# Optimization experiments

Hardware: AMD Instinct MI355X
Metric: run time of the kernel (lower is better)

Reference implementation:

```python
import jax, jax.numpy as jnp
import numpy as np

D_MODEL = 1024
N_HEADS = 16
HEAD_DIM = D_MODEL // N_HEADS


def setup_inputs() -> dict:
    key = jax.random.key(0)
    ks = jax.random.split(key, 11)
    B, S = 4, 2048
    scale = 1.0 / np.sqrt(D_MODEL)
    inp = {
        "query": jax.random.normal(ks[0], (B, S, D_MODEL), jnp.float32),
        "key": jax.random.normal(ks[1], (B, S, D_MODEL), jnp.float32),
        "value": jax.random.normal(ks[2], (B, S, D_MODEL), jnp.float32),
        "Wq": jax.random.normal(ks[3], (D_MODEL, D_MODEL), jnp.float32) * scale,
        "bq": jnp.zeros((D_MODEL,), jnp.float32),
        "Wk": jax.random.normal(ks[4], (D_MODEL, D_MODEL), jnp.float32) * scale,
        "bk": jnp.zeros((D_MODEL,), jnp.float32),
        "Wv": jax.random.normal(ks[5], (D_MODEL, D_MODEL), jnp.float32) * scale,
        "bv": jnp.zeros((D_MODEL,), jnp.float32),
        "Wo": jax.random.normal(ks[6], (D_MODEL, D_MODEL), jnp.float32) * scale,
        "bo": jnp.zeros((D_MODEL,), jnp.float32),
    }
    return inp


def reference(query, key, value, Wq, bq, Wk, bk, Wv, bv, Wo, bo):
    B, S, _ = query.shape
    # QKV projections (nn.Linear: x @ W.T + b; weights here stored as [out,in])
    q = query @ Wq.T + bq
    k = key @ Wk.T + bk
    v = value @ Wv.T + bv
    # [B, S, H, Dh] -> [B, H, S, Dh]
    q = q.reshape(B, S, N_HEADS, HEAD_DIM).transpose(0, 2, 1, 3)
    k = k.reshape(B, S, N_HEADS, HEAD_DIM).transpose(0, 2, 1, 3)
    v = v.reshape(B, S, N_HEADS, HEAD_DIM).transpose(0, 2, 1, 3)
    # full score matrix [B, H, S, S]
    scores = jnp.einsum("bhqd,bhkd->bhqk", q, k) / jnp.sqrt(
        jnp.asarray(HEAD_DIM, q.dtype)
    )
    attn = jax.nn.softmax(scores, axis=-1)
    out = jnp.einsum("bhqk,bhkd->bhqd", attn, v)  # [B, H, S, Dh]
    out = out.transpose(0, 2, 1, 3).reshape(B, S, D_MODEL)
    return out @ Wo.T + bo
```

## Files before the change

kernel.cpp:

```cpp
#include <hip/hip_runtime.h>
#include <cstdint>
#include <cstddef>


typedef _Float16 h16;
typedef _Float16 h16x4 __attribute__((ext_vector_type(4)));
typedef _Float16 h16x8 __attribute__((ext_vector_type(8)));
typedef float f32x4 __attribute__((ext_vector_type(4)));
typedef float f32x16 __attribute__((ext_vector_type(16)));

#define SEQ 2048
#define HDIM 64

__device__ __forceinline__ void gld16(const void* g, void* l) {
  __builtin_amdgcn_global_load_lds((__attribute__((address_space(1))) void*)g,
                                   (__attribute__((address_space(3))) void*)l,
                                   16, 0, 0);
}

struct CvtArgs {
  const float* src[7];
  h16* dst[7];
  int n4[7];
};

__global__ __launch_bounds__(256) void cvt_kernel(CvtArgs a) {
  const int tk = blockIdx.y;
  const int n4 = a.n4[tk];
  const float4* s = (const float4*)a.src[tk];
  h16x4* d = (h16x4*)a.dst[tk];
  const int stride = gridDim.x * blockDim.x;
  for (int i = blockIdx.x * blockDim.x + threadIdx.x; i < n4; i += stride) {
    float4 v = s[i];
    h16x4 o = {(h16)v.x, (h16)v.y, (h16)v.z, (h16)v.w};
    d[i] = o;
  }
}

enum { EPI_QK = 0, EPI_V = 1, EPI_OUT = 2 };

struct GemmArgs {
  const h16* A[3];
  const h16* W[3];
  const float* bias[3];
  void* dst[3];
  float scale[3];
  int epi[3];
};

__global__ __launch_bounds__(256) void gemm_h16(GemmArgs g) {
  const int z = blockIdx.z;
  const h16* A = g.A[z];
  const h16* W = g.W[z];
  const float* bias = g.bias[z];
  void* dst = g.dst[z];
  const float scale = g.scale[z];
  const int epi = g.epi[z];

  __shared__ __align__(16) h16 sA[128 * 32];
  __shared__ __align__(16) h16 sW[128 * 32];

  const int t = threadIdx.x;
  const int lane = t & 63, wave = t >> 6;
  const int lq = lane & 15, quad = lane >> 4;
  const int wm = wave & 1, wn = wave >> 1;
  const int m0 = blockIdx.y * 128, n0 = blockIdx.x * 128;

  const int srow = wave * 32 + (lane >> 2);
  const int scol = (lane & 3) * 8;
  const h16* Ag = A + (size_t)(m0 + srow) * 1024 + scol;
  const h16* Wg = W + (size_t)(n0 + srow) * 1024 + scol;
  h16* lA = &sA[(wave * 32) * 32];
  h16* lW = &sW[(wave * 32) * 32];

  f32x4 zero4 = {0.f, 0.f, 0.f, 0.f};
  f32x4 acc[4][4];
#pragma unroll
  for (int i = 0; i < 4; ++i)
#pragma unroll
    for (int j = 0; j < 4; ++j) acc[i][j] = zero4;

  for (int k0 = 0; k0 < 1024; k0 += 32) {
    __syncthreads();
    gld16(Ag + k0, lA);
    gld16(Ag + k0 + 16 * 1024, lA + 16 * 32);
    gld16(Wg + k0, lW);
    gld16(Wg + k0 + 16 * 1024, lW + 16 * 32);
    __syncthreads();

    h16x8 af[4], wf[4];
#pragma unroll
    for (int mt = 0; mt < 4; ++mt)
      af[mt] = *(const h16x8*)&sA[(wm * 64 + mt * 16 + lq) * 32 + quad * 8];
#pragma unroll
    for (int nt = 0; nt < 4; ++nt)
      wf[nt] = *(const h16x8*)&sW[(wn * 64 + nt * 16 + lq) * 32 + quad * 8];
#pragma unroll
    for (int mt = 0; mt < 4; ++mt)
#pragma unroll
      for (int nt = 0; nt < 4; ++nt)
        acc[mt][nt] = __builtin_amdgcn_mfma_f32_16x16x32_f16(
            af[mt], wf[nt], acc[mt][nt], 0, 0, 0);
  }

  const int gmb = m0 + wm * 64;
  const int gnb = n0 + wn * 64;
#pragma unroll
  for (int mt = 0; mt < 4; ++mt) {
#pragma unroll
    for (int nt = 0; nt < 4; ++nt) {
      const int gn = gnb + nt * 16 + lq;
      const float bv = bias[gn];
#pragma unroll
      for (int r = 0; r < 4; ++r) {
        const int gm = gmb + mt * 16 + quad * 4 + r;
        const float v = (acc[mt][nt][r] + bv) * scale;
        if (epi == EPI_OUT) {
          ((float*)dst)[(size_t)gm * 1024 + gn] = v;
        } else if (epi == EPI_QK) {
          const int b = gm >> 11, s = gm & 2047, h = gn >> 6, d = gn & 63;
          ((h16*)dst)[((size_t)(b * 16 + h) * 2048 + s) * 64 + d] = (h16)v;
        } else {
          const int b = gm >> 11, s = gm & 2047, h = gn >> 6, d = gn & 63;
          ((h16*)dst)[((size_t)(b * 16 + h) * 64 + d) * 2048 + s] = (h16)v;
        }
      }
    }
  }
}

__global__ __launch_bounds__(256, 4) void flash_fwd(
    const h16* __restrict__ Qp, const h16* __restrict__ Kp,
    const h16* __restrict__ Vtp, h16* __restrict__ attn) {
  __shared__ __align__(16) h16 sK[128 * 72];
  __shared__ __align__(16) h16 sVt[64 * 136];

  const int t = threadIdx.x, lane = t & 63, wave = t >> 6;
  const int l31 = lane & 31;
  const int h = lane >> 5;
  const int bh = blockIdx.y, q0 = blockIdx.x * 128;

  const h16* Qh = Qp + (size_t)bh * SEQ * HDIM;
  const h16* Kh = Kp + (size_t)bh * SEQ * HDIM;
  const h16* Vh = Vtp + (size_t)bh * HDIM * SEQ;

  const int qrow = q0 + wave * 32 + l31;
  h16x8 bq[4];
#pragma unroll
  for (int ks = 0; ks < 4; ++ks)
    bq[ks] = *(const h16x8*)(Qh + (size_t)qrow * 64 + ks * 16 + h * 8);

  f32x16 zero16 = {};
  f32x16 oT[2];
  oT[0] = zero16;
  oT[1] = zero16;
  float lsum = 0.f;

  for (int kt = 0; kt < SEQ; kt += 128) {
    __syncthreads();
#pragma unroll
    for (int p = 0; p < 4; ++p) {
      const int c = t + p * 256;
      const int rowK = c >> 3, colK = (c & 7) * 8;
      *(h16x8*)&sK[rowK * 72 + colK] =
          *(const h16x8*)(Kh + (size_t)(kt + rowK) * 64 + colK);
      const int rowV = c >> 4, colV = (c & 15) * 8;
      *(h16x8*)&sVt[rowV * 136 + colV] =
          *(const h16x8*)(Vh + (size_t)rowV * SEQ + kt + colV);
    }
    __syncthreads();

    uint2 pk[16];
#pragma unroll
    for (int mt = 0; mt < 4; ++mt) {
      f32x16 s = zero16;
#pragma unroll
      for (int ks = 0; ks < 4; ++ks) {
        h16x8 ak = *(const h16x8*)&sK[(mt * 32 + l31) * 72 + ks * 16 + h * 8];
        s = __builtin_amdgcn_mfma_f32_32x32x16_f16(ak, bq[ks], s, 0, 0, 0);
      }
#pragma unroll
      for (int g = 0; g < 4; ++g) {
        const float p0 = __expf(s[g * 4 + 0]);
        const float p1 = __expf(s[g * 4 + 1]);
        const float p2 = __expf(s[g * 4 + 2]);
        const float p3 = __expf(s[g * 4 + 3]);
        lsum += (p0 + p1) + (p2 + p3);
        h16x4 q4 = {(h16)p0, (h16)p1, (h16)p2, (h16)p3};
        pk[mt * 4 + g] = __builtin_bit_cast(uint2, q4);
      }
    }

#pragma unroll
    for (int ks = 0; ks < 8; ++ks) {
      const uint2 a = pk[2 * ks];
      const uint2 b = pk[2 * ks + 1];
      uint2 send;
      send.x = h ? a.x : b.x;
      send.y = h ? a.y : b.y;
      uint2 recv;
      recv.x = (unsigned)__shfl_xor((int)send.x, 32);
      recv.y = (unsigned)__shfl_xor((int)send.y, 32);
      uint2 lo, hi;
      lo.x = h ? recv.x : a.x;
      lo.y = h ? recv.y : a.y;
      hi.x = h ? b.x : recv.x;
      hi.y = h ? b.y : recv.y;
      uint4 bp32 = {lo.x, lo.y, hi.x, hi.y};
      h16x8 bp = __builtin_bit_cast(h16x8, bp32);
#pragma unroll
      for (int dt = 0; dt < 2; ++dt) {
        h16x8 av =
            *(const h16x8*)&sVt[(dt * 32 + l31) * 136 + ks * 16 + h * 8];
        oT[dt] = __builtin_amdgcn_mfma_f32_32x32x16_f16(av, bp, oT[dt], 0, 0, 0);
      }
    }
  }

  lsum += __shfl_xor(lsum, 32);
  const float inv = 1.f / lsum;

  const int b = bh >> 4, head = bh & 15;
  h16* orow = attn + ((size_t)(b * SEQ + qrow)) * 1024 + head * 64;
#pragma unroll
  for (int dt = 0; dt < 2; ++dt) {
#pragma unroll
    for (int g = 0; g < 4; ++g) {
      h16x4 ov = {(h16)(oT[dt][g * 4 + 0] * inv), (h16)(oT[dt][g * 4 + 1] * inv),
                  (h16)(oT[dt][g * 4 + 2] * inv), (h16)(oT[dt][g * 4 + 3] * inv)};
      *(h16x4*)&orow[dt * 32 + g * 8 + h * 4] = ov;
    }
  }
}

extern "C" void kernel_launch(void* const* d_in, const int* in_sizes, int n_in,
                              void* d_out, int out_size, void* d_ws,
                              size_t ws_size, hipStream_t stream) {
  (void)in_sizes; (void)n_in; (void)out_size;

  const float* query = (const float*)d_in[0];
  const float* key   = (const float*)d_in[1];
  const float* value = (const float*)d_in[2];
  const float* Wq = (const float*)d_in[3];
  const float* bq = (const float*)d_in[4];
  const float* Wk = (const float*)d_in[5];
  const float* bk = (const float*)d_in[6];
  const float* Wv = (const float*)d_in[7];
  const float* bv = (const float*)d_in[8];
  const float* Wo = (const float*)d_in[9];
  const float* bo = (const float*)d_in[10];

  char* ws = (char*)d_ws;
  const size_t MB = 1024 * 1024;
  h16* xq = (h16*)(ws);
  h16* xk = (h16*)(ws + 16 * MB);
  h16* xv = (h16*)(ws + 32 * MB);
  h16* qperm = (h16*)(ws + 48 * MB);
  h16 *kperm, *vperm, *attn, *w16;
  const bool fused = ws_size >= 104 * MB;
  if (fused) {
    kperm = (h16*)(ws + 64 * MB);
    vperm = (h16*)(ws + 80 * MB);
    w16   = (h16*)(ws + 96 * MB);
    attn  = (h16*)(ws);
  } else {
    kperm = (h16*)(ws);
    vperm = (h16*)(ws + 16 * MB);
    attn  = (h16*)(ws + 32 * MB);
    w16   = (h16*)(ws + 64 * MB);
  }
  h16* wq16 = w16;
  h16* wk16 = w16 + 1048576;
  h16* wv16 = w16 + 2 * 1048576;
  h16* wo16 = w16 + 3 * 1048576;

  CvtArgs ca;
  const float* csrc[7] = {query, key, value, Wq, Wk, Wv, Wo};
  h16* cdst[7] = {xq, xk, xv, wq16, wk16, wv16, wo16};
  const int cn4[7] = {2097152, 2097152, 2097152, 262144, 262144, 262144, 262144};
  for (int i = 0; i < 7; ++i) { ca.src[i] = csrc[i]; ca.dst[i] = cdst[i]; ca.n4[i] = cn4[i]; }
  cvt_kernel<<<dim3(512, 7), 256, 0, stream>>>(ca);

  if (fused) {
    GemmArgs ga;
    ga.A[0] = xq; ga.A[1] = xk; ga.A[2] = xv;
    ga.W[0] = wq16; ga.W[1] = wk16; ga.W[2] = wv16;
    ga.bias[0] = bq; ga.bias[1] = bk; ga.bias[2] = bv;
    ga.dst[0] = qperm; ga.dst[1] = kperm; ga.dst[2] = vperm;
    ga.scale[0] = 0.125f; ga.scale[1] = 1.f; ga.scale[2] = 1.f;
    ga.epi[0] = EPI_QK; ga.epi[1] = EPI_QK; ga.epi[2] = EPI_V;
    gemm_h16<<<dim3(8, 64, 3), 256, 0, stream>>>(ga);
  } else {
    const h16* As[3] = {xq, xk, xv};
    const h16* Ws[3] = {wq16, wk16, wv16};
    const float* bs[3] = {bq, bk, bv};
    h16* ds[3] = {qperm, kperm, vperm};
    const float scl[3] = {0.125f, 1.f, 1.f};
    const int ep[3] = {EPI_QK, EPI_QK, EPI_V};
    for (int i = 0; i < 3; ++i) {
      GemmArgs ga;
      for (int j = 0; j < 3; ++j) {
        ga.A[j] = As[i]; ga.W[j] = Ws[i]; ga.bias[j] = bs[i];
        ga.dst[j] = ds[i]; ga.scale[j] = scl[i]; ga.epi[j] = ep[i];
      }
      gemm_h16<<<dim3(8, 64, 1), 256, 0, stream>>>(ga);
    }
  }

  flash_fwd<<<dim3(16, 64), 256, 0, stream>>>(qperm, kperm, vperm, attn);

  GemmArgs go;
  for (int j = 0; j < 3; ++j) {
    go.A[j] = attn; go.W[j] = wo16; go.bias[j] = bo;
    go.dst[j] = d_out; go.scale[j] = 1.f; go.epi[j] = EPI_OUT;
  }
  gemm_h16<<<dim3(8, 64, 1), 256, 0, stream>>>(go);
}
```

Before: 394.3 us.

## Replace GEMM with 256x256-tile, 4-stage pipelined, swizzled LDS kernel

Swaps the 128x128 single-buffered projection GEMM for a 256x256 tile kernel with 512 threads. It uses a 4-slot LDS ring of async global-to-LDS loads (three stages in flight, waited on with vmcnt), an XOR-swizzled LDS layout against bank conflicts, block-id remapping for L2 locality, and setprio around the MFMA bursts. The aim is to hide load latency and raise arithmetic intensity. In exchange it needs 128KB of dynamic LDS, has fewer blocks (128 per GEMM) on a 256-CU device, and carries hand-tuned waitcnt logic that is fragile.

```diff
diff --git a/kernel.cpp b/kernel.cpp
--- a/kernel.cpp
+++ b/kernel.cpp
@@ -17,6 +17,9 @@
                                    (__attribute__((address_space(3))) void*)l,
                                    16, 0, 0);
 }
+
+#define VMCNT_(n) asm volatile("s_waitcnt vmcnt(" #n ")" ::: "memory")
+#define VMCNT(n) VMCNT_(n)
 
 struct CvtArgs {
   const float* src[7];
@@ -48,73 +51,126 @@
   int epi[3];
 };
 
-__global__ __launch_bounds__(256) void gemm_h16(GemmArgs g) {
+__global__ __launch_bounds__(512, 2) void gemm256(GemmArgs g) {
+  extern __shared__ __align__(16) h16 lds[];
+
   const int z = blockIdx.z;
-  const h16* A = g.A[z];
-  const h16* W = g.W[z];
-  const float* bias = g.bias[z];
+  const h16* __restrict__ A = g.A[z];
+  const h16* __restrict__ W = g.W[z];
+  const float* __restrict__ bias = g.bias[z];
   void* dst = g.dst[z];
   const float scale = g.scale[z];
   const int epi = g.epi[z];
 
-  __shared__ __align__(16) h16 sA[128 * 32];
-  __shared__ __align__(16) h16 sW[128 * 32];
+  int bid = blockIdx.y * 4 + blockIdx.x;
+  bid = (bid & 7) * 16 + (bid >> 3);
+  const int m0 = (bid >> 2) * 256;
+  const int n0 = (bid & 3) * 256;
 
   const int t = threadIdx.x;
   const int lane = t & 63, wave = t >> 6;
   const int lq = lane & 15, quad = lane >> 4;
-  const int wm = wave & 1, wn = wave >> 1;
-  const int m0 = blockIdx.y * 128, n0 = blockIdx.x * 128;
-
-  const int srow = wave * 32 + (lane >> 2);
-  const int scol = (lane & 3) * 8;
-  const h16* Ag = A + (size_t)(m0 + srow) * 1024 + scol;
-  const h16* Wg = W + (size_t)(n0 + srow) * 1024 + scol;
-  h16* lA = &sA[(wave * 32) * 32];
-  h16* lW = &sW[(wave * 32) * 32];
-
+  const int wm = wave >> 2, wn = wave & 3;
+
+  const int l2 = lane >> 2;
+  const int qsw = (lane & 3) ^ ((lane >> 3) & 3);
+  const h16* gA0 = A + (size_t)(m0 + (wave * 2 + 0) * 16 + l2) * 1024 + qsw * 8;
+  const h16* gA1 = A + (size_t)(m0 + (wave * 2 + 1) * 16 + l2) * 1024 + qsw * 8;
+  const h16* gB0 = W + (size_t)(n0 + (wave * 2 + 0) * 16 + l2) * 1024 + qsw * 8;
+  const h16* gB1 = W + (size_t)(n0 + (wave * 2 + 1) * 16 + l2) * 1024 + qsw * 8;
+  h16* ldsA0 = &lds[(wave * 2 + 0) * 512];
+  h16* ldsA1 = &lds[(wave * 2 + 1) * 512];
+  h16* ldsB0 = &lds[8192 + (wave * 2 + 0) * 512];
+  h16* ldsB1 = &lds[8192 + (wave * 2 + 1) * 512];
+
+  const int swr = quad ^ ((lq >> 1) & 3);
+  const int aRd = (wm * 128 + lq) * 32 + swr * 8;
+  const int bRd = 8192 + (wn * 64 + lq) * 32 + swr * 8;
+
+  f32x4 acc[8][4];
   f32x4 zero4 = {0.f, 0.f, 0.f, 0.f};
-  f32x4 acc[4][4];
-#pragma unroll
-  for (int i = 0; i < 4; ++i)
+#pragma unroll
+  for (int i = 0; i < 8; ++i)
 #pragma unroll
     for (int j = 0; j < 4; ++j) acc[i][j] = zero4;
 
-  for (int k0 = 0; k0 < 1024; k0 += 32) {
-    __syncthreads();
-    gld16(Ag + k0, lA);
-    gld16(Ag + k0 + 16 * 1024, lA + 16 * 32);
-    gld16(Wg + k0, lW);
-    gld16(Wg + k0 + 16 * 1024, lW + 16 * 32);
-    __syncthreads();
-
-    h16x8 af[4], wf[4];
-#pragma unroll
-    for (int mt = 0; mt < 4; ++mt)
-      af[mt] = *(const h16x8*)&sA[(wm * 64 + mt * 16 + lq) * 32 + quad * 8];
-#pragma unroll
-    for (int nt = 0; nt < 4; ++nt)
-      wf[nt] = *(const h16x8*)&sW[(wn * 64 + nt * 16 + lq) * 32 + quad * 8];
-#pragma unroll
-    for (int mt = 0; mt < 4; ++mt)
-#pragma unroll
-      for (int nt = 0; nt < 4; ++nt)
-        acc[mt][nt] = __builtin_amdgcn_mfma_f32_16x16x32_f16(
-            af[mt], wf[nt], acc[mt][nt], 0, 0, 0);
-  }
-
-  const int gmb = m0 + wm * 64;
+#pragma unroll
+  for (int s = 0; s < 3; ++s) {
+    gld16(gA0 + s * 32, ldsA0 + s * 16384);
+    gld16(gB0 + s * 32, ldsB0 + s * 16384);
+    gld16(gA1 + s * 32, ldsA1 + s * 16384);
+    gld16(gB1 + s * 32, ldsB1 + s * 16384);
+  }
+
+#define SUBTILE(SLOT, STK, DO_STAGE, VM)                                      \
+  {                                                                           \
+    VMCNT(VM);                                                                \
+    __builtin_amdgcn_s_barrier();                                             \
+    __builtin_amdgcn_sched_barrier(0);                                        \
+    const h16* aS = &lds[(SLOT) * 16384 + aRd];                               \
+    const h16* bS = &lds[(SLOT) * 16384 + bRd];                               \
+    h16x8 af0[4], bf[4], af1[4];                                              \
+    _Pragma("unroll") for (int i = 0; i < 4; ++i) {                           \
+      af0[i] = *(const h16x8*)(aS + i * 512);                                 \
+    }                                                                         \
+    _Pragma("unroll") for (int i = 0; i < 4; ++i) {                           \
+      bf[i] = *(const h16x8*)(bS + i * 512);                                  \
+    }                                                                         \
+    if (DO_STAGE) {                                                           \
+      gld16(gA0 + (STK), ldsA0 + ((SLOT + 3) & 3) * 16384);                   \
+      gld16(gB0 + (STK), ldsB0 + ((SLOT + 3) & 3) * 16384);                   \
+    }                                                                         \
+    __builtin_amdgcn_s_setprio(1);                                            \
+    _Pragma("unroll") for (int i = 0; i < 4; ++i) {                           \
+      _Pragma("unroll") for (int j = 0; j < 4; ++j) {                         \
+        acc[i][j] = __builtin_amdgcn_mfma_f32_16x16x32_f16(af0[i], bf[j],     \
+                                                           acc[i][j], 0, 0, 0);\
+      }                                                                       \
+    }                                                                         \
+    __builtin_amdgcn_s_setprio(0);                                            \
+    _Pragma("unroll") for (int i = 0; i < 4; ++i) {                           \
+      af1[i] = *(const h16x8*)(aS + (4 + i) * 512);                           \
+    }                                                                         \
+    if (DO_STAGE) {                                                           \
+      gld16(gA1 + (STK), ldsA1 + ((SLOT + 3) & 3) * 16384);                   \
+      gld16(gB1 + (STK), ldsB1 + ((SLOT + 3) & 3) * 16384);                   \
+    }                                                                         \
+    __builtin_amdgcn_s_setprio(1);                                            \
+    _Pragma("unroll") for (int i = 0; i < 4; ++i) {                           \
+      _Pragma("unroll") for (int j = 0; j < 4; ++j) {                         \
+        acc[4 + i][j] = __builtin_amdgcn_mfma_f32_16x16x32_f16(               \
+            af1[i], bf[j], acc[4 + i][j], 0, 0, 0);                           \
+      }                                                                       \
+    }                                                                         \
+    __builtin_amdgcn_s_setprio(0);                                            \
+  }
+
+  int kb = 0;
+#pragma unroll 1
+  for (int s4 = 0; s4 < 7; ++s4, kb += 128) {
+    SUBTILE(0, kb + 96, true, 8);
+    SUBTILE(1, kb + 128, true, 8);
+    SUBTILE(2, kb + 160, true, 8);
+    SUBTILE(3, kb + 192, true, 8);
+  }
+  SUBTILE(0, 992, true, 8);
+  SUBTILE(1, 0, false, 8);
+  SUBTILE(2, 0, false, 4);
+  SUBTILE(3, 0, false, 0);
+#undef SUBTILE
+
+  const int gmb = m0 + wm * 128;
   const int gnb = n0 + wn * 64;
 #pragma unroll
-  for (int mt = 0; mt < 4; ++mt) {
-#pragma unroll
-    for (int nt = 0; nt < 4; ++nt) {
-      const int gn = gnb + nt * 16 + lq;
+  for (int mf = 0; mf < 8; ++mf) {
+#pragma unroll
+    for (int nf = 0; nf < 4; ++nf) {
+      const int gn = gnb + nf * 16 + lq;
       const float bv = bias[gn];
 #pragma unroll
       for (int r = 0; r < 4; ++r) {
-        const int gm = gmb + mt * 16 + quad * 4 + r;
-        const float v = (acc[mt][nt][r] + bv) * scale;
+        const int gm = gmb + mf * 16 + quad * 4 + r;
+        const float v = (acc[mf][nf][r] + bv) * scale;
         if (epi == EPI_OUT) {
           ((float*)dst)[(size_t)gm * 1024 + gn] = v;
         } else if (epi == EPI_QK) {
@@ -274,6 +330,14 @@
   h16* wv16 = w16 + 2 * 1048576;
   h16* wo16 = w16 + 3 * 1048576;
 
+  static bool attr_set = false;
+  if (!attr_set) {
+    (void)hipFuncSetAttribute((const void*)gemm256,
+                              hipFuncAttributeMaxDynamicSharedMemorySize,
+                              131072);
+    attr_set = true;
+  }
+
   CvtArgs ca;
   const float* csrc[7] = {query, key, value, Wq, Wk, Wv, Wo};
   h16* cdst[7] = {xq, xk, xv, wq16, wk16, wv16, wo16};
@@ -289,7 +353,7 @@
     ga.dst[0] = qperm; ga.dst[1] = kperm; ga.dst[2] = vperm;
     ga.scale[0] = 0.125f; ga.scale[1] = 1.f; ga.scale[2] = 1.f;
     ga.epi[0] = EPI_QK; ga.epi[1] = EPI_QK; ga.epi[2] = EPI_V;
-    gemm_h16<<<dim3(8, 64, 3), 256, 0, stream>>>(ga);
+    gemm256<<<dim3(4, 32, 3), 512, 131072, stream>>>(ga);
   } else {
     const h16* As[3] = {xq, xk, xv};
     const h16* Ws[3] = {wq16, wk16, wv16};
@@ -303,7 +367,7 @@
         ga.A[j] = As[i]; ga.W[j] = Ws[i]; ga.bias[j] = bs[i];
         ga.dst[j] = ds[i]; ga.scale[j] = scl[i]; ga.epi[j] = ep[i];
       }
-      gemm_h16<<<dim3(8, 64, 1), 256, 0, stream>>>(ga);
+      gemm256<<<dim3(4, 32, 1), 512, 131072, stream>>>(ga);
     }
   }
 
@@ -314,5 +378,5 @@
     go.A[j] = attn; go.W[j] = wo16; go.bias[j] = bo;
     go.dst[j] = d_out; go.scale[j] = 1.f; go.epi[j] = EPI_OUT;
   }
-  gemm_h16<<<dim3(8, 64, 1), 256, 0, stream>>>(go);
-}
+  gemm256<<<dim3(4, 32, 1), 512, 131072, stream>>>(go);
+}
```

Measured after the change: 408.8 us. 1.04x slower.
